# Kernel tuning notes

Hardware: AMD Instinct MI355X
Metric: run time of the kernel (lower is better)

The kernel has to match this reference:

```python
import jax, jax.numpy as jnp
import numpy as np

B, S, D, H, DFF = 4, 2048, 1024, 16, 4096
HD = D // H
EPS = 1e-12

def _layernorm(x, g, b):
    mu = jnp.mean(x, axis=-1, keepdims=True)
    var = jnp.mean(jnp.square(x - mu), axis=-1, keepdims=True)
    return (x - mu) * jax.lax.rsqrt(var + EPS) * g + b

def setup_inputs() -> dict:
    key = jax.random.key(0)
    ks = jax.random.split(key, 12)
    sd = 0.02
    inp = {
        'hidden_states': jax.random.normal(ks[0], (B, S, D), jnp.float32),
        'attention_mask': jnp.zeros((B, 1, 1, S), jnp.float32),
        'Wq': jax.random.normal(ks[1], (D, D), jnp.float32) * sd,
        'bq': jnp.zeros((D,), jnp.float32),
        'Wk': jax.random.normal(ks[2], (D, D), jnp.float32) * sd,
        'bk': jnp.zeros((D,), jnp.float32),
        'Wv': jax.random.normal(ks[3], (D, D), jnp.float32) * sd,
        'bv': jnp.zeros((D,), jnp.float32),
        'Wo': jax.random.normal(ks[4], (D, D), jnp.float32) * sd,
        'bo': jnp.zeros((D,), jnp.float32),
        'ln1_g': jnp.ones((D,), jnp.float32),
        'ln1_b': jnp.zeros((D,), jnp.float32),
        'Wi': jax.random.normal(ks[5], (D, DFF), jnp.float32) * sd,
        'bi': jnp.zeros((DFF,), jnp.float32),
        'Wo2': jax.random.normal(ks[6], (DFF, D), jnp.float32) * sd,
        'bo2': jnp.zeros((D,), jnp.float32),
        'ln2_g': jnp.ones((D,), jnp.float32),
        'ln2_b': jnp.zeros((D,), jnp.float32),
    }
    return inp

def reference(hidden_states, attention_mask, Wq, bq, Wk, bk, Wv, bv, Wo, bo,
              ln1_g, ln1_b, Wi, bi, Wo2, bo2, ln2_g, ln2_b):
    x = hidden_states  # [B,S,D]
    # project and split heads -> [B,H,S,hd]
    def heads(t):
        return t.reshape(B, S, H, HD).transpose(0, 2, 1, 3)
    q = heads(x @ Wq + bq)
    k = heads(x @ Wk + bk)
    v = heads(x @ Wv + bv)
    scores = jnp.einsum('bhqd,bhkd->bhqk', q, k) / np.float32(np.sqrt(HD))
    scores = scores + attention_mask  # additive mask broadcast [B,1,1,S]
    weights = jax.nn.softmax(scores, axis=-1)
    ctx = jnp.einsum('bhqk,bhkd->bhqd', weights, v)
    ctx = ctx.transpose(0, 2, 1, 3).reshape(B, S, D)
    attn_out = _layernorm(ctx @ Wo + bo + x, ln1_g, ln1_b)
    # FFN (gelu) with residual + LayerNorm
    h = jax.nn.gelu(attn_out @ Wi + bi, approximate=False)
    out = _layernorm(h @ Wo2 + bo2 + attn_out, ln2_g, ln2_b)
    return out
```

## Files before the change

kernel.cpp:

```cpp
#include <hip/hip_runtime.h>
#include <hip/hip_bf16.h>
#include <math.h>

#define B_   4
#define S_   2048
#define D_   1024
#define H_   16
#define HD_  64
#define DFF_ 4096
#define M_   (B_*S_)

typedef __bf16 bf16x8 __attribute__((ext_vector_type(8)));
typedef __bf16 bf16x4 __attribute__((ext_vector_type(4)));
typedef float  floatx4 __attribute__((ext_vector_type(4)));

__device__ __forceinline__ float  b2f(__bf16 v) { return (float)v; }
__device__ __forceinline__ __bf16 f2b(float v)  { return (__bf16)v; }

__device__ __forceinline__ void async_ld16(const void* g, void* l) {
    __builtin_amdgcn_global_load_lds(
        (const __attribute__((address_space(1))) unsigned int*)g,
        (__attribute__((address_space(3))) unsigned int*)l, 16, 0, 0);
}

__global__ __launch_bounds__(256)
void prep_kernel(const float* __restrict__ Wq, const float* __restrict__ Wk,
                 const float* __restrict__ Wv, const float* __restrict__ Wo,
                 const float* __restrict__ Wi, const float* __restrict__ Wo2,
                 const float* __restrict__ bq, const float* __restrict__ bk,
                 const float* __restrict__ bv, const float* __restrict__ hid,
                 __bf16* __restrict__ wqkvb, __bf16* __restrict__ wob,
                 __bf16* __restrict__ wib, __bf16* __restrict__ wo2b,
                 float* __restrict__ qkvbias, __bf16* __restrict__ hb)
{
    __shared__ float t[32][33];
    const int bid = blockIdx.x;
    const int tid = threadIdx.x;

    if (bid < 12288) {
        const float* in; __bf16* outp; int R, C, nx, lid; float scale = 1.0f;
        if (bid < 1024)      { in = Wq;  outp = wqkvb;           R = D_;   C = D_;   nx = 32;  lid = bid;        scale = 0.125f; }
        else if (bid < 2048) { in = Wk;  outp = wqkvb + D_*D_;   R = D_;   C = D_;   nx = 32;  lid = bid - 1024; }
        else if (bid < 3072) { in = Wv;  outp = wqkvb + 2*D_*D_; R = D_;   C = D_;   nx = 32;  lid = bid - 2048; }
        else if (bid < 4096) { in = Wo;  outp = wob;             R = D_;   C = D_;   nx = 32;  lid = bid - 3072; }
        else if (bid < 8192) { in = Wi;  outp = wib;             R = D_;   C = DFF_; nx = 128; lid = bid - 4096; }
        else                 { in = Wo2; outp = wo2b;            R = DFF_; C = D_;   nx = 32;  lid = bid - 8192; }
        const int c0 = (lid % nx) * 32, r0 = (lid / nx) * 32;
        const int tx = tid & 31, ty = tid >> 5;
        for (int i = ty; i < 32; i += 8)
            t[i][tx] = in[(long)(r0 + i) * C + c0 + tx];
        __syncthreads();
        for (int i = ty; i < 32; i += 8)
            outp[(long)(c0 + i) * R + r0 + tx] = f2b(t[tx][i] * scale);
    } else if (bid < 16384) {
        long i = ((long)(bid - 12288) * 256 + tid) * 8;
        if (i >= (long)M_ * D_) return;
        float4 a = *(const float4*)&hid[i];
        float4 c = *(const float4*)&hid[i + 4];
        union { __bf16 h[8]; uint4 u; } p;
        p.h[0] = f2b(a.x); p.h[1] = f2b(a.y); p.h[2] = f2b(a.z); p.h[3] = f2b(a.w);
        p.h[4] = f2b(c.x); p.h[5] = f2b(c.y); p.h[6] = f2b(c.z); p.h[7] = f2b(c.w);
        *(uint4*)&hb[i] = p.u;
    } else {
        int i = (bid - 16384) * 256 + tid;
        if (i >= 3 * D_) return;
        float v = (i < D_) ? bq[i] * 0.125f
                : (i < 2 * D_) ? bk[i - D_] : bv[i - 2 * D_];
        qkvbias[i] = v;
    }
}

__global__ void vt_transpose_kernel(const __bf16* __restrict__ qkv,
                                    __bf16* __restrict__ vtg)
{
    __shared__ __bf16 t[32][34];
    int b  = blockIdx.z;
    int h  = blockIdx.y >> 1;
    int d0 = (blockIdx.y & 1) * 32;
    int s0 = blockIdx.x * 32;
    int tx = threadIdx.x, ty = threadIdx.y;
    for (int i = ty; i < 32; i += 8)
        t[i][tx] = qkv[(long)(b * S_ + s0 + i) * 3072 + 2048 + h * 64 + d0 + tx];
    __syncthreads();
    for (int i = ty; i < 32; i += 8)
        vtg[((long)(b * H_ + h) * 64 + d0 + i) * S_ + s0 + tx] = t[tx][i];
}

template<int MODE>
__global__ __launch_bounds__(256, 2)
void gemm_kernel(const __bf16* __restrict__ A, const __bf16* __restrict__ Bt,
                 const float* __restrict__ bias, const float* __restrict__ resid,
                 float* __restrict__ Cf, __bf16* __restrict__ Cb,
                 int M, int N, int K)
{
    __shared__ __bf16 sA[128 * 64];
    __shared__ __bf16 sB[128 * 64];

    const int tid  = threadIdx.x;
    const int lane = tid & 63;
    const int wave = tid >> 6;
    const int wm   = (wave >> 1) * 64;
    const int wn   = (wave & 1) * 64;
    const long bm  = (long)blockIdx.y * 128;
    const long bn  = (long)blockIdx.x * 128;

    floatx4 acc[4][4];
#pragma unroll
    for (int i = 0; i < 4; ++i)
#pragma unroll
        for (int j = 0; j < 4; ++j)
#pragma unroll
            for (int r = 0; r < 4; ++r) acc[i][j][r] = 0.0f;

    const int mrow = lane & 15;
    const int quad = lane >> 4;
    const int koff0 = ((0 * 4 + quad) ^ (mrow & 7)) * 8;
    const int koff1 = ((1 * 4 + quad) ^ (mrow & 7)) * 8;

    for (int k0 = 0; k0 < K; k0 += 64) {
        __syncthreads();
#pragma unroll
        for (int t = 0; t < 4; ++t) {
            int ci  = tid + t * 256;
            int row = ci >> 3;
            int col = ((ci & 7) ^ (row & 7)) << 3;
            async_ld16(A  + (bm + row) * (long)K + k0 + col, &sA[ci * 8]);
            async_ld16(Bt + (bn + row) * (long)K + k0 + col, &sB[ci * 8]);
        }
        __syncthreads();

#pragma unroll
        for (int s = 0; s < 2; ++s) {
            const int ko = s ? koff1 : koff0;
            bf16x8 a[4], b[4];
#pragma unroll
            for (int i = 0; i < 4; ++i)
                a[i] = *(const bf16x8*)&sA[(wm + i * 16 + mrow) * 64 + ko];
#pragma unroll
            for (int j = 0; j < 4; ++j)
                b[j] = *(const bf16x8*)&sB[(wn + j * 16 + mrow) * 64 + ko];
#pragma unroll
            for (int i = 0; i < 4; ++i)
#pragma unroll
                for (int j = 0; j < 4; ++j)
                    acc[i][j] = __builtin_amdgcn_mfma_f32_16x16x32_bf16(
                        a[i], b[j], acc[i][j], 0, 0, 0);
        }
    }

    const int rq = quad * 4;
    const int cn = lane & 15;
#pragma unroll
    for (int i = 0; i < 4; ++i) {
#pragma unroll
        for (int j = 0; j < 4; ++j) {
            long col = bn + wn + j * 16 + cn;
            float bv = bias[col];
#pragma unroll
            for (int r = 0; r < 4; ++r) {
                long row = bm + wm + i * 16 + rq + r;
                float v = acc[i][j][r] + bv;
                if (MODE == 0) {
                    Cb[row * N + col] = f2b(v);
                } else if (MODE == 1) {
                    Cf[row * N + col] = v + resid[row * N + col];
                } else {
                    float g = 0.5f * v * (1.0f + erff(v * 0.70710678118654752f));
                    Cb[row * N + col] = f2b(g);
                }
            }
        }
    }
}

__global__ __launch_bounds__(512, 2)
void attn_kernel(const __bf16* __restrict__ QKV, const __bf16* __restrict__ VT,
                 const float* __restrict__ mask, __bf16* __restrict__ ctx)
{
    __shared__ __bf16 Ks[2][64 * 64];
    __shared__ __bf16 Vt[2][64 * 64];
    __shared__ __bf16 Ps[2][64 * 64];

    const int tid  = threadIdx.x;
    const int lane = tid & 63;
    const int wave = tid >> 6;
    const int qh   = wave >> 2;
    const int w16  = (wave & 3) * 16;

    const int ibk  = blockIdx.x;
    const int xcd  = ibk & 7;
    const int tt   = ibk >> 3;
    const int head_lin = xcd * 8 + (tt >> 4);
    const int q0   = (tt & 15) * 128;
    const int b    = head_lin >> 4;
    const int h    = head_lin & 15;

    const int cn   = lane & 15;
    const int quad = lane >> 4;
    const int rq   = quad * 4;
    const int koff0 = ((0 * 4 + quad) ^ (cn & 7)) * 8;
    const int koff1 = ((1 * 4 + quad) ^ (cn & 7)) * 8;

    const long vbase = ((long)(b * H_ + h) * 64) * S_;
    __bf16* PsAll = &Ps[0][0];

    auto STAGE = [&](int bufi, int k0) {
        int ci = tid;
        int r  = ci >> 3;
        int cz = ((ci & 7) ^ (r & 7)) << 3;
        async_ld16(QKV + (long)(b * S_ + k0 + r) * 3072 + 1024 + h * 64 + cz,
                   &Ks[bufi][ci * 8]);
        async_ld16(VT + vbase + (long)r * S_ + k0 + cz, &Vt[bufi][ci * 8]);
    };

#pragma unroll
    for (int t = 0; t < 2; ++t) {
        int ci = tid + t * 512;
        int qr = ci >> 3;
        int dc = ((ci & 7) ^ (qr & 7)) << 3;
        async_ld16(QKV + (long)(b * S_ + q0 + qr) * 3072 + h * 64 + dc,
                   &PsAll[ci * 8]);
    }
    STAGE(0, 0);
    float mv[4];
#pragma unroll
    for (int jt = 0; jt < 4; ++jt)
        mv[jt] = mask[(long)b * S_ + jt * 16 + cn] - 8.0f;
    asm volatile("s_waitcnt vmcnt(0)" ::: "memory");
    __builtin_amdgcn_s_barrier();
    __builtin_amdgcn_sched_barrier(0);

    const bf16x8 aq0 = *(const bf16x8*)&Ps[qh][(w16 + cn) * 64 + koff0];
    const bf16x8 aq1 = *(const bf16x8*)&Ps[qh][(w16 + cn) * 64 + koff1];

    float l_[4];
    floatx4 o_[4];
#pragma unroll
    for (int r = 0; r < 4; ++r) l_[r] = 0.0f;
#pragma unroll
    for (int jt = 0; jt < 4; ++jt)
#pragma unroll
        for (int r = 0; r < 4; ++r) o_[jt][r] = 0.0f;

    int cur = 0;
    for (int k0 = 0; k0 < S_; k0 += 64) {
        float mvn[4];
        if (k0 + 64 < S_) {
            STAGE(cur ^ 1, k0 + 64);
#pragma unroll
            for (int jt = 0; jt < 4; ++jt)
                mvn[jt] = mask[(long)b * S_ + k0 + 64 + jt * 16 + cn] - 8.0f;
        }

        floatx4 st[4];
#pragma unroll
        for (int jt = 0; jt < 4; ++jt)
#pragma unroll
            for (int r = 0; r < 4; ++r) st[jt][r] = 0.0f;
        __builtin_amdgcn_s_setprio(1);
#pragma unroll
        for (int jt = 0; jt < 4; ++jt) {
            bf16x8 b0 = *(const bf16x8*)&Ks[cur][(jt * 16 + cn) * 64 + koff0];
            bf16x8 b1 = *(const bf16x8*)&Ks[cur][(jt * 16 + cn) * 64 + koff1];
            st[jt] = __builtin_amdgcn_mfma_f32_16x16x32_bf16(aq0, b0, st[jt], 0, 0, 0);
            st[jt] = __builtin_amdgcn_mfma_f32_16x16x32_bf16(aq1, b1, st[jt], 0, 0, 0);
        }
        __builtin_amdgcn_s_setprio(0);
#pragma unroll
        for (int jt = 0; jt < 4; ++jt) {
#pragma unroll
            for (int r = 0; r < 4; ++r) {
                float p = __expf(st[jt][r] + mv[jt]);
                st[jt][r] = p;
                l_[r] += p;
            }
        }
#pragma unroll
        for (int jt = 0; jt < 4; ++jt)
#pragma unroll
            for (int r = 0; r < 4; ++r) {
                int prow = w16 + rq + r;
                int pcol = (((jt * 2 + (cn >> 3)) ^ (prow & 7)) << 3) + (cn & 7);
                Ps[qh][prow * 64 + pcol] = f2b(st[jt][r]);
            }

        {
            bf16x8 ap0 = *(const bf16x8*)&Ps[qh][(w16 + cn) * 64 + koff0];
            bf16x8 ap1 = *(const bf16x8*)&Ps[qh][(w16 + cn) * 64 + koff1];
            __builtin_amdgcn_s_setprio(1);
#pragma unroll
            for (int jt = 0; jt < 4; ++jt) {
                bf16x8 b0 = *(const bf16x8*)&Vt[cur][(jt * 16 + cn) * 64 + koff0];
                bf16x8 b1 = *(const bf16x8*)&Vt[cur][(jt * 16 + cn) * 64 + koff1];
                o_[jt] = __builtin_amdgcn_mfma_f32_16x16x32_bf16(ap0, b0, o_[jt], 0, 0, 0);
                o_[jt] = __builtin_amdgcn_mfma_f32_16x16x32_bf16(ap1, b1, o_[jt], 0, 0, 0);
            }
            __builtin_amdgcn_s_setprio(0);
        }

        asm volatile("s_waitcnt vmcnt(0) lgkmcnt(0)" ::: "memory");
        __builtin_amdgcn_s_barrier();
        __builtin_amdgcn_sched_barrier(0);
        if (k0 + 64 < S_) {
#pragma unroll
            for (int jt = 0; jt < 4; ++jt) mv[jt] = mvn[jt];
        }
        cur ^= 1;
    }

#pragma unroll
    for (int r = 0; r < 4; ++r) {
        float l = l_[r];
        l += __shfl_xor(l, 1);
        l += __shfl_xor(l, 2);
        l += __shfl_xor(l, 4);
        l += __shfl_xor(l, 8);
        float linv = 1.0f / l;
        long rowg = (long)(b * S_ + q0 + qh * 64 + w16 + rq + r) * D_ + h * 64;
#pragma unroll
        for (int jt = 0; jt < 4; ++jt)
            ctx[rowg + jt * 16 + cn] = f2b(o_[jt][r] * linv);
    }
}

__global__ __launch_bounds__(256)
void ln_kernel(const float* __restrict__ X, const float* __restrict__ gamma,
               const float* __restrict__ beta, float* __restrict__ out,
               __bf16* __restrict__ outb)
{
    const long row = blockIdx.x;
    const int tid = threadIdx.x;
    const float* x = X + row * D_;
    float4 v = *(const float4*)&x[tid * 4];
    float s  = v.x + v.y + v.z + v.w;
    float s2 = v.x * v.x + v.y * v.y + v.z * v.z + v.w * v.w;
    for (int off = 32; off > 0; off >>= 1) {
        s  += __shfl_down(s, off);
        s2 += __shfl_down(s2, off);
    }
    __shared__ float red[8];
    int wave = tid >> 6, lane = tid & 63;
    if (lane == 0) { red[wave] = s; red[4 + wave] = s2; }
    __syncthreads();
    float ts  = red[0] + red[1] + red[2] + red[3];
    float ts2 = red[4] + red[5] + red[6] + red[7];
    float mu  = ts * (1.0f / D_);
    float var = ts2 * (1.0f / D_) - mu * mu;
    float rs  = rsqrtf(fmaxf(var, 0.0f) + 1e-12f);
    float4 g = *(const float4*)&gamma[tid * 4];
    float4 b = *(const float4*)&beta[tid * 4];
    float4 o;
    o.x = (v.x - mu) * rs * g.x + b.x;
    o.y = (v.y - mu) * rs * g.y + b.y;
    o.z = (v.z - mu) * rs * g.z + b.z;
    o.w = (v.w - mu) * rs * g.w + b.w;
    *(float4*)&out[row * D_ + tid * 4] = o;
    if (outb) {
        bf16x4 ob;
        ob[0] = f2b(o.x); ob[1] = f2b(o.y); ob[2] = f2b(o.z); ob[3] = f2b(o.w);
        *(bf16x4*)&outb[row * D_ + tid * 4] = ob;
    }
}

extern "C" void kernel_launch(void* const* d_in, const int* in_sizes, int n_in,
                              void* d_out, int out_size, void* d_ws, size_t ws_size,
                              hipStream_t stream)
{
    const float* hid  = (const float*)d_in[0];
    const float* mask = (const float*)d_in[1];
    const float* Wq   = (const float*)d_in[2];
    const float* bq   = (const float*)d_in[3];
    const float* Wk   = (const float*)d_in[4];
    const float* bk   = (const float*)d_in[5];
    const float* Wv   = (const float*)d_in[6];
    const float* bv   = (const float*)d_in[7];
    const float* Wo   = (const float*)d_in[8];
    const float* bo   = (const float*)d_in[9];
    const float* g1   = (const float*)d_in[10];
    const float* b1   = (const float*)d_in[11];
    const float* Wi   = (const float*)d_in[12];
    const float* bi   = (const float*)d_in[13];
    const float* Wo2  = (const float*)d_in[14];
    const float* bo2  = (const float*)d_in[15];
    const float* g2   = (const float*)d_in[16];
    const float* b2   = (const float*)d_in[17];
    float* out = (float*)d_out;

    char* w = (char*)d_ws;
    auto take = [&](size_t bytes) { char* p = w; w += bytes; return p; };
    __bf16* wqkvb = (__bf16*)take((size_t)3 * D_ * D_ * 2);
    __bf16* wob   = (__bf16*)take((size_t)D_ * D_ * 2);
    __bf16* wib   = (__bf16*)take((size_t)D_ * DFF_ * 2);
    __bf16* wo2b  = (__bf16*)take((size_t)D_ * DFF_ * 2);
    float*  qkvbias = (float*)take(16384);
    __bf16* qkv   = (__bf16*)take((size_t)M_ * 3 * D_ * 2);
    __bf16* ctxb  = (__bf16*)take((size_t)M_ * D_ * 2);
    __bf16* hb    = (__bf16*)take((size_t)M_ * D_ * 2);
    float*  tmp      = (float*)take((size_t)M_ * D_ * 4);
    float*  attn_out = (float*)take((size_t)M_ * D_ * 4);
    __bf16* hbuf = qkv;
    __bf16* vtg  = hb;
    __bf16* attn_out_b = hb;
    (void)in_sizes; (void)n_in; (void)out_size; (void)ws_size;

    prep_kernel<<<16396, 256, 0, stream>>>(
        Wq, Wk, Wv, Wo, Wi, Wo2, bq, bk, bv, hid,
        wqkvb, wob, wib, wo2b, qkvbias, hb);

    gemm_kernel<0><<<dim3(3*D_/128, M_/128), 256, 0, stream>>>(
        hb, wqkvb, qkvbias, nullptr, nullptr, qkv, M_, 3*D_, D_);

    dim3 tb(32, 8);
    vt_transpose_kernel<<<dim3(S_/32, H_*2, B_), tb, 0, stream>>>(qkv, vtg);

    attn_kernel<<<1024, 512, 0, stream>>>(qkv, vtg, mask, ctxb);

    gemm_kernel<1><<<dim3(D_/128, M_/128), 256, 0, stream>>>(
        ctxb, wob, bo, hid, tmp, nullptr, M_, D_, D_);
    ln_kernel<<<M_, 256, 0, stream>>>(tmp, g1, b1, attn_out, attn_out_b);

    gemm_kernel<2><<<dim3(DFF_/128, M_/128), 256, 0, stream>>>(
        attn_out_b, wib, bi, nullptr, nullptr, hbuf, M_, DFF_, D_);
    gemm_kernel<1><<<dim3(D_/128, M_/128), 256, 0, stream>>>(
        hbuf, wo2b, bo2, attn_out, tmp, nullptr, M_, D_, DFF_);
    ln_kernel<<<M_, 256, 0, stream>>>(tmp, g2, b2, out, nullptr);
}
```

Baseline: 548.6 us.

## Fuse V transpose into QKV GEMM epilogue and remap workgroups across XCDs

Drops the separate V-transpose kernel. The QKV GEMM epilogue now writes the V columns directly into a transposed [B,H,64,S] buffer, packing 4 consecutive rows as a uint2 store. The transposed V buffer moves into the fp32 tmp scratch so it does not alias the bf16 input still being read. Workgroup IDs are also remapped so that blocks dispatched to the same XCD get contiguous tiles, improving L2 locality. The price is an extra strided epilogue store per V tile and a grid size that must be divisible by 8.

```diff
diff --git a/kernel.cpp b/kernel.cpp
--- a/kernel.cpp
+++ b/kernel.cpp
@@ -70,27 +70,12 @@
     }
 }
 
-__global__ void vt_transpose_kernel(const __bf16* __restrict__ qkv,
-                                    __bf16* __restrict__ vtg)
-{
-    __shared__ __bf16 t[32][34];
-    int b  = blockIdx.z;
-    int h  = blockIdx.y >> 1;
-    int d0 = (blockIdx.y & 1) * 32;
-    int s0 = blockIdx.x * 32;
-    int tx = threadIdx.x, ty = threadIdx.y;
-    for (int i = ty; i < 32; i += 8)
-        t[i][tx] = qkv[(long)(b * S_ + s0 + i) * 3072 + 2048 + h * 64 + d0 + tx];
-    __syncthreads();
-    for (int i = ty; i < 32; i += 8)
-        vtg[((long)(b * H_ + h) * 64 + d0 + i) * S_ + s0 + tx] = t[tx][i];
-}
-
 template<int MODE>
 __global__ __launch_bounds__(256, 2)
 void gemm_kernel(const __bf16* __restrict__ A, const __bf16* __restrict__ Bt,
                  const float* __restrict__ bias, const float* __restrict__ resid,
                  float* __restrict__ Cf, __bf16* __restrict__ Cb,
+                 __bf16* __restrict__ vtg,
                  int M, int N, int K)
 {
     __shared__ __bf16 sA[128 * 64];
@@ -101,8 +86,13 @@
     const int wave = tid >> 6;
     const int wm   = (wave >> 1) * 64;
     const int wn   = (wave & 1) * 64;
-    const long bm  = (long)blockIdx.y * 128;
-    const long bn  = (long)blockIdx.x * 128;
+
+    const int nbx = gridDim.x;
+    const int nwg = nbx * gridDim.y;
+    const int orig = blockIdx.y * nbx + blockIdx.x;
+    const int wg = (orig & 7) * (nwg >> 3) + (orig >> 3);
+    const long bm = (long)(wg / nbx) * 128;
+    const long bn = (long)(wg % nbx) * 128;
 
     floatx4 acc[4][4];
 #pragma unroll
@@ -156,18 +146,29 @@
         for (int j = 0; j < 4; ++j) {
             long col = bn + wn + j * 16 + cn;
             float bv = bias[col];
+            union { __bf16 h[4]; uint2 u2; } pk;
 #pragma unroll
             for (int r = 0; r < 4; ++r) {
                 long row = bm + wm + i * 16 + rq + r;
                 float v = acc[i][j][r] + bv;
                 if (MODE == 0) {
-                    Cb[row * N + col] = f2b(v);
+                    __bf16 bvv = f2b(v);
+                    Cb[row * N + col] = bvv;
+                    pk.h[r] = bvv;
                 } else if (MODE == 1) {
                     Cf[row * N + col] = v + resid[row * N + col];
                 } else {
                     float g = 0.5f * v * (1.0f + erff(v * 0.70710678118654752f));
                     Cb[row * N + col] = f2b(g);
                 }
+            }
+            if (MODE == 0 && vtg != nullptr && col >= 2048) {
+                long row0 = bm + wm + i * 16 + rq;
+                int bb = (int)(row0 >> 11);
+                int ss = (int)(row0 & 2047);
+                int hh = ((int)col - 2048) >> 6;
+                int dd = ((int)col - 2048) & 63;
+                *(uint2*)&vtg[((long)(bb * H_ + hh) * 64 + dd) * S_ + ss] = pk.u2;
             }
         }
     }
@@ -399,7 +400,7 @@
     float*  tmp      = (float*)take((size_t)M_ * D_ * 4);
     float*  attn_out = (float*)take((size_t)M_ * D_ * 4);
     __bf16* hbuf = qkv;
-    __bf16* vtg  = hb;
+    __bf16* vtg  = (__bf16*)tmp;
     __bf16* attn_out_b = hb;
     (void)in_sizes; (void)n_in; (void)out_size; (void)ws_size;
 
@@ -408,20 +409,17 @@
         wqkvb, wob, wib, wo2b, qkvbias, hb);
 
     gemm_kernel<0><<<dim3(3*D_/128, M_/128), 256, 0, stream>>>(
-        hb, wqkvb, qkvbias, nullptr, nullptr, qkv, M_, 3*D_, D_);
-
-    dim3 tb(32, 8);
-    vt_transpose_kernel<<<dim3(S_/32, H_*2, B_), tb, 0, stream>>>(qkv, vtg);
+        hb, wqkvb, qkvbias, nullptr, nullptr, qkv, vtg, M_, 3*D_, D_);
 
     attn_kernel<<<1024, 512, 0, stream>>>(qkv, vtg, mask, ctxb);
 
     gemm_kernel<1><<<dim3(D_/128, M_/128), 256, 0, stream>>>(
-        ctxb, wob, bo, hid, tmp, nullptr, M_, D_, D_);
+        ctxb, wob, bo, hid, tmp, nullptr, nullptr, M_, D_, D_);
     ln_kernel<<<M_, 256, 0, stream>>>(tmp, g1, b1, attn_out, attn_out_b);
 
     gemm_kernel<2><<<dim3(DFF_/128, M_/128), 256, 0, stream>>>(
-        attn_out_b, wib, bi, nullptr, nullptr, hbuf, M_, DFF_, D_);
+        attn_out_b, wib, bi, nullptr, nullptr, hbuf, nullptr, M_, DFF_, D_);
     gemm_kernel<1><<<dim3(D_/128, M_/128), 256, 0, stream>>>(
-        hbuf, wo2b, bo2, attn_out, tmp, nullptr, M_, D_, DFF_);
+        hbuf, wo2b, bo2, attn_out, tmp, nullptr, nullptr, M_, D_, DFF_);
     ln_kernel<<<M_, 256, 0, stream>>>(tmp, g2, b2, out, nullptr);
 }
```

Measured after the change: 551.9 us. About the same (+0.6%).
